# Optimization experiments

Hardware: AMD Instinct MI355X
Metric: run time of the kernel (lower is better)

Reference implementation:

```python
import jax, jax.numpy as jnp
import numpy as np

D_MODEL = 768
BATCH = 4096
RANK_DIST = [(4, 512), (8, 256), (16, 128), (32, 64), (64, 32)]


@jax.custom_vjp
def jumprelu(x):
    # hard threshold at 0 in fwd; full straight-through estimator in bwd
    return x * (x > 0.0).astype(x.dtype)


def _jr_fwd(x):
    return jumprelu(x), None


def _jr_bwd(res, g):
    return (g,)


jumprelu.defvjp(_jr_fwd, _jr_bwd)


def setup_inputs() -> dict:
    key = jax.random.key(0)
    keys = jax.random.split(key, 1 + 3 * len(RANK_DIST))
    inp = {"x": jax.random.normal(keys[0], (BATCH, D_MODEL), dtype=jnp.float32)}
    for i, (n, r) in enumerate(RANK_DIST):
        kV, kU, kE = keys[1 + 3 * i], keys[2 + 3 * i], keys[3 + 3 * i]
        scale = (1.0 / (D_MODEL * r)) ** 0.25
        inp[f"V{i}"] = scale * jax.random.normal(kV, (n, r, D_MODEL), dtype=jnp.float32)
        inp[f"U{i}"] = scale * jax.random.normal(kU, (n, D_MODEL, r), dtype=jnp.float32)
        enc = jax.random.normal(kE, (n, D_MODEL), dtype=jnp.float32)
        inp[f"enc{i}"] = enc / jnp.linalg.norm(enc, axis=1, keepdims=True)
        inp[f"b{i}"] = jnp.full((n,), -1.0, dtype=jnp.float32)
    return inp


def _group_forward(x, V, U, enc, b):
    n, r, d = V.shape
    pre = x @ enc.T - b                      # (b, n)
    gate = jumprelu(pre)                     # (b, n)
    Vx = jnp.einsum("nrd,bd->nbr", V, x)    # (n, b, r)
    # fused: UVx gated by gate then summed over transforms n
    out = jnp.einsum("ndr,nbr,bn->bd", U, Vx, gate)  # (b, d)
    u_norms = jnp.linalg.norm(U.reshape(n, -1), axis=1)
    v_norms = jnp.linalg.norm(V.reshape(n, -1), axis=1)
    frob = u_norms * v_norms / jnp.sqrt(jnp.asarray(d * r, dtype=x.dtype))
    return out, gate, frob


def reference(x, V0, U0, enc0, b0, V1, U1, enc1, b1, V2, U2, enc2, b2,
              V3, U3, enc3, b3, V4, U4, enc4, b4):
    Vs = [V0, V1, V2, V3, V4]
    Us = [U0, U1, U2, U3, U4]
    encs = [enc0, enc1, enc2, enc3, enc4]
    bs = [b0, b1, b2, b3, b4]
    output = jnp.zeros_like(x)
    total_sparsity = jnp.asarray(0.0, dtype=x.dtype)
    total_active = jnp.asarray(0.0, dtype=x.dtype)
    gate_acts = []
    for V, U, enc, b in zip(Vs, Us, encs, bs):
        g_out, gate, frob = _group_forward(x, V, U, enc, b)
        output = output + g_out
        mean_abs_gate = jnp.abs(gate).mean(axis=0)
        total_sparsity = total_sparsity + (jnp.tanh(mean_abs_gate) * frob).sum()
        total_active = total_active + (gate > 0).astype(x.dtype).sum(axis=1).mean()
        gate_acts.append(gate)
    return (output, total_sparsity, total_active, *gate_acts)
```

## Files before the change

### kernel.cpp

```cpp
#include <hip/hip_runtime.h>

#define BATCH 4096
#define DM 768
#define LTOT 10240
#define NG 124

typedef __bf16 bf16x8 __attribute__((ext_vector_type(8)));
typedef short short8 __attribute__((ext_vector_type(8)));
typedef float f32x4 __attribute__((ext_vector_type(4)));

struct Ptr5 { const float* p[5]; };

__device__ __forceinline__ unsigned short f2bf(float f) {
    unsigned u = __builtin_bit_cast(unsigned, f);
    unsigned r = (u + 0x7FFFu + ((u >> 16) & 1u)) >> 16;
    return (unsigned short)r;
}

__device__ __forceinline__ short8 pack8(float4 a, float4 b) {
    union { unsigned short u[8]; short8 s; } o;
    o.u[0] = f2bf(a.x); o.u[1] = f2bf(a.y); o.u[2] = f2bf(a.z); o.u[3] = f2bf(a.w);
    o.u[4] = f2bf(b.x); o.u[5] = f2bf(b.y); o.u[6] = f2bf(b.z); o.u[7] = f2bf(b.w);
    return o.s;
}


__global__ __launch_bounds__(256) void prep_k(const float* __restrict__ x,
                                              Ptr5 vp, Ptr5 up, Ptr5 ep, Ptr5 bp,
                                              unsigned short* __restrict__ vb,
                                              unsigned short* __restrict__ w2t,
                                              unsigned short* __restrict__ xb,
                                              float* __restrict__ gate_ws,
                                              float* __restrict__ outg,
                                              float* __restrict__ vslot,
                                              float* __restrict__ uslot,
                                              float* __restrict__ gslot,
                                              float* __restrict__ aslot) {
    const int basen[5] = {0, 4, 12, 28, 60};
    int bx = blockIdx.x;
    int tid = threadIdx.x;
    if (bx < 32) {
        __shared__ unsigned short lA[128 * 64];
        __shared__ unsigned short lB[128 * 64];
        __shared__ float sgs[128];
        __shared__ float sac;
        int wave = tid >> 6, lane = tid & 63;
        int wm = wave >> 1, wn = wave & 1;
        int lan15 = lane & 15, quad = lane >> 4;
        int sw = lan15 & 7;
        int m0 = bx * 128;
        f32x4 acc[4][4] = {};
        for (int k0 = 0; k0 < DM; k0 += 64) {
            __syncthreads();
            #pragma unroll
            for (int i = 0; i < 4; i++) {
                int gidx = i * 256 + tid;
                int row = gidx >> 3, kb = gidx & 7;
                int r7 = row & 7;
                int la = (row >> 3) * 512 + r7 * 64 + (kb ^ r7) * 8;
                int sidx = (m0 + row) * 192 + (k0 >> 2) + kb * 2;
                float4 a0 = ((const float4*)x)[sidx];
                float4 a1 = ((const float4*)x)[sidx + 1];
                *(short8*)(lA + la) = pack8(a0, a1);
                float4 b0 = {0.f, 0.f, 0.f, 0.f}, b1 = {0.f, 0.f, 0.f, 0.f};
                if (row < NG) {
                    int g = (row < 4) ? 0 : (row < 12) ? 1 : (row < 28) ? 2 :
                            (row < 60) ? 3 : 4;
                    int ni = row - basen[g];
                    int eidx = ni * 192 + (k0 >> 2) + kb * 2;
                    b0 = ((const float4*)ep.p[g])[eidx];
                    b1 = ((const float4*)ep.p[g])[eidx + 1];
                }
                *(short8*)(lB + la) = pack8(b0, b1);
            }
            __syncthreads();
            #pragma unroll
            for (int kk = 0; kk < 2; kk++) {
                int kb = kk * 4 + quad;
                int kel = (kb ^ sw) * 8;
                bf16x8 af[4], bfr[4];
                #pragma unroll
                for (int t = 0; t < 4; t++) {
                    short8 ra = *(const short8*)(lA + (wm * 64 + t * 16 + lan15) * 64 + kel);
                    short8 rb = *(const short8*)(lB + (wn * 64 + t * 16 + lan15) * 64 + kel);
                    af[t]  = __builtin_bit_cast(bf16x8, ra);
                    bfr[t] = __builtin_bit_cast(bf16x8, rb);
                }
                #pragma unroll
                for (int mt = 0; mt < 4; mt++)
                    #pragma unroll
                    for (int nt = 0; nt < 4; nt++)
                        acc[mt][nt] = __builtin_amdgcn_mfma_f32_16x16x32_bf16(
                            af[mt], bfr[nt], acc[mt][nt], 0, 0, 0);
            }
        }
        if (tid < 128) sgs[tid] = 0.f;
        if (tid == 0) sac = 0.f;
        __syncthreads();
        const size_t baseg[5] = {3145730ull, 3145730ull + 16384, 3145730ull + 49152,
                                 3145730ull + 114688, 3145730ull + 245760};
        float cnt = 0.f;
        #pragma unroll
        for (int nt = 0; nt < 4; nt++) {
            int col = wn * 64 + nt * 16 + lan15;
            float cs = 0.f;
            if (col < NG) {
                int g = (col < 4) ? 0 : (col < 12) ? 1 : (col < 28) ? 2 :
                        (col < 60) ? 3 : 4;
                int ni = col - basen[g];
                int w = 4 << g;
                float bv = bp.p[g][ni];
                #pragma unroll
                for (int mt = 0; mt < 4; mt++) {
                    int r0 = m0 + wm * 64 + mt * 16 + quad * 4;
                    #pragma unroll
                    for (int rg = 0; rg < 4; rg++) {
                        float pre = acc[mt][nt][rg] - bv;
                        float gt = pre > 0.f ? pre : 0.f;
                        gate_ws[(size_t)(r0 + rg) * NG + col] = gt;
                        outg[baseg[g] + (size_t)(r0 + rg) * w + ni] = gt;
                        cs += gt;
                        if (pre > 0.f) cnt += 1.f;
                    }
                }
                cs += __shfl_xor(cs, 16);
                cs += __shfl_xor(cs, 32);
                if (quad == 0) atomicAdd(&sgs[col], cs);
            }
        }
        #pragma unroll
        for (int off = 32; off > 0; off >>= 1) cnt += __shfl_xor(cnt, off);
        if (lane == 0) atomicAdd(&sac, cnt);
        __syncthreads();
        if (tid < NG) gslot[bx * NG + tid] = sgs[tid];
        if (tid == 0) aslot[bx] = sac;
    } else if (bx < 1952) {
        __shared__ float swave[4];
        int cb = bx - 32;
        int isV = cb < 960;
        int wb = isV ? cb : cb - 960;
        int g = wb / 192;
        int within = wb - g * 192;
        const float* src = isV ? vp.p[g] : up.p[g];
        int r = 512 >> g, lr = 9 - g;
        float ss = 0.f;
        #pragma unroll
        for (int i = 0; i < 8; i++) {
            int j = within * 2048 + i * 256 + tid;
            float4 v = ((const float4*)src)[j];
            ss += v.x*v.x + v.y*v.y + v.z*v.z + v.w*v.w;
            ushort4 o;
            o.x = f2bf(v.x); o.y = f2bf(v.y); o.z = f2bf(v.z); o.w = f2bf(v.w);
            if (isV) {
                ((ushort4*)vb)[(size_t)(g * 192 + within) * 2048 + i * 256 + tid] = o;
            } else {
                int idx = j * 4;
                int rr = idx & (r - 1);
                int t2 = idx >> lr;
                int d  = t2 % DM;
                int n  = t2 / DM;
                size_t dst = (size_t)d * LTOT + (size_t)(g << 11) + (size_t)n * r + rr;
                *(ushort4*)(w2t + dst) = o;
            }
        }
        #pragma unroll
        for (int off = 32; off > 0; off >>= 1) ss += __shfl_down(ss, off);
        if ((tid & 63) == 0) swave[tid >> 6] = ss;
        __syncthreads();
        if (tid == 0) {
            float t = (swave[0] + swave[1]) + (swave[2] + swave[3]);
            (isV ? vslot : uslot)[wb] = t;
        }
    } else {
        int base = (bx - 1952) * 2048;
        #pragma unroll
        for (int i = 0; i < 8; i++) {
            int j = base + i * 256 + tid;
            float4 v = ((const float4*)x)[j];
            ushort4 o;
            o.x = f2bf(v.x); o.y = f2bf(v.y); o.z = f2bf(v.z); o.w = f2bf(v.w);
            ((ushort4*)xb)[j] = o;
        }
    }
}

template <int ROWS, int NT>
__device__ __forceinline__ void stage(const unsigned short* __restrict__ src, int ld,
                                      unsigned short* lds, int wv, int lane) {
    int rsub = lane >> 3;
    int colb = ((lane ^ rsub) & 7) * 8;
    #pragma unroll
    for (int i = 0; i < ROWS * 8 / NT; i++) {
        int c = i * (NT / 64) + wv;
        const unsigned short* gp = src + (size_t)(c * 8 + rsub) * ld + colb;
        __builtin_amdgcn_global_load_lds((const __attribute__((address_space(1))) void*)gp,
                                         (__attribute__((address_space(3))) void*)(lds + c * 512),
                                         16, 0, 0);
    }
}

template <int BM, int BN, int NT>
__global__ __launch_bounds__(NT) void gemm_nt(const unsigned short* __restrict__ A,
                                              const unsigned short* __restrict__ Bm,
                                              int Kblk, int lda, int ldb,
                                              void* __restrict__ Cout,
                                              const float* __restrict__ gate, int ldc) {
    __shared__ unsigned short lA[BM * 64];
    __shared__ unsigned short lB[BN * 64];
    int tid = threadIdx.x, wave = tid >> 6, lane = tid & 63;
    constexpr int WN = BN / 64;
    int wm = wave / WN, wn = wave % WN;
    int m0 = blockIdx.x * BM, n0 = blockIdx.y * BN;
    A  += (size_t)m0 * lda;
    Bm += (size_t)n0 * ldb;
    f32x4 acc[4][4] = {};
    int lan15 = lane & 15, quad = lane >> 4;
    int sw = lan15 & 7;

    for (int k0 = 0; k0 < Kblk; k0 += 64) {
        stage<BM, NT>(A + k0, lda, lA, wave, lane);
        stage<BN, NT>(Bm + k0, ldb, lB, wave, lane);
        __syncthreads();
        #pragma unroll
        for (int kk = 0; kk < 2; kk++) {
            int kb = kk * 4 + quad;
            int kel = (kb ^ sw) * 8;
            bf16x8 af[4], bfr[4];
            #pragma unroll
            for (int t = 0; t < 4; t++) {
                short8 ra = *(const short8*)(lA + (size_t)(wm * 64 + t * 16 + lan15) * 64 + kel);
                short8 rb = *(const short8*)(lB + (size_t)(wn * 64 + t * 16 + lan15) * 64 + kel);
                af[t]  = __builtin_bit_cast(bf16x8, ra);
                bfr[t] = __builtin_bit_cast(bf16x8, rb);
            }
            #pragma unroll
            for (int mt = 0; mt < 4; mt++)
                #pragma unroll
                for (int nt = 0; nt < 4; nt++)
                    acc[mt][nt] = __builtin_amdgcn_mfma_f32_16x16x32_bf16(af[mt], bfr[nt],
                                                                          acc[mt][nt], 0, 0, 0);
        }
        __syncthreads();
    }

    const int basen[5] = {0, 4, 12, 28, 60};
    unsigned short* H = (unsigned short*)Cout;
    #pragma unroll
    for (int mt = 0; mt < 4; mt++) {
        __syncthreads();
        #pragma unroll
        for (int nt = 0; nt < 4; nt++) {
            int col = n0 + wn * 64 + nt * 16 + lan15;
            int g = col >> 11;
            int ngl = basen[g] + ((col & 2047) >> (9 - g));
            #pragma unroll
            for (int rg = 0; rg < 4; rg++) {
                int grow = m0 + wm * 64 + mt * 16 + quad * 4 + rg;
                float gv = gate[(size_t)grow * NG + ngl];
                lA[wave * 1024 + (quad * 4 + rg) * 64 + nt * 16 + lan15] =
                    f2bf(acc[mt][nt][rg] * gv);
            }
        }
        __syncthreads();
        #pragma unroll
        for (int i = 0; i < 2; i++) {
            int f = i * NT + tid;
            int R = f >> 5;
            int u = f & 31;
            int wv2 = ((R >> 4) << 2) + (u >> 3);
            short8 vread = *(const short8*)(lA + wv2 * 1024 + (R & 15) * 64 + (u & 7) * 8);
            int grow = m0 + (R >> 4) * 64 + mt * 16 + (R & 15);
            *(short8*)(H + (size_t)grow * ldc + n0 + u * 8) = vread;
        }
    }
}

__global__ __launch_bounds__(512, 1) void gemm2_nt(const unsigned short* __restrict__ A,
                                                   const unsigned short* __restrict__ Bm,
                                                   float* __restrict__ P) {
    __shared__ unsigned short lds[65536];
    const int tid = threadIdx.x;
    const int wave = tid >> 6, lane = tid & 63;
    const int wm = wave >> 2, wn = wave & 3;
    const int lan15 = lane & 15, quad = lane >> 4;
    const int swz = quad ^ ((lan15 >> 1) & 3);
    const int m0 = blockIdx.x * 256, n0 = blockIdx.y * 256;
    const unsigned short* Ab = A  + (size_t)m0 * LTOT + blockIdx.z * 2048;
    const unsigned short* Bb = Bm + (size_t)n0 * LTOT + blockIdx.z * 2048;
    const int srow = lane >> 2;
    const int sgr  = (lane & 3) ^ ((lane >> 3) & 3);
    const int rdA = (wm * 128 + lan15) * 32 + swz * 8;
    const int rdB = 32768 + (wn * 64 + lan15) * 32 + swz * 8;

#define STG(base_us, gb, koff) do { \
    const unsigned short* _s0 = (gb) + (size_t)(wave * 16 + srow) * LTOT + (koff) + sgr * 8; \
    const unsigned short* _s1 = (gb) + (size_t)((wave + 8) * 16 + srow) * LTOT + (koff) + sgr * 8; \
    __builtin_amdgcn_global_load_lds((const __attribute__((address_space(1))) void*)_s0, \
        (__attribute__((address_space(3))) void*)(lds + (base_us) + wave * 512), 16, 0, 0); \
    __builtin_amdgcn_global_load_lds((const __attribute__((address_space(1))) void*)_s1, \
        (__attribute__((address_space(3))) void*)(lds + (base_us) + (wave + 8) * 512), 16, 0, 0); \
} while (0)
#define STGA(buf, kh, koff) STG(((buf) * 2 + (kh)) * 8192, Ab, koff)
#define STGB(buf, kh, koff) STG(32768 + ((buf) * 2 + (kh)) * 8192, Bb, koff)

#define RDA(msub, bufkg) { \
    _Pragma("unroll") for (int t = 0; t < 4; t++) \
        af[t] = __builtin_bit_cast(bf16x8, \
            *(const short8*)(lds + (bufkg) * 8192 + rdA + ((msub) * 64 + t * 16) * 32)); }
#define RDB(bufkg) { \
    _Pragma("unroll") for (int t = 0; t < 4; t++) \
        bf[t] = __builtin_bit_cast(bf16x8, \
            *(const short8*)(lds + 32768 + (bufkg) * 8192 + rdB - 32768 + t * 512)); }
#define SYNC1 do { __builtin_amdgcn_s_barrier(); \
    asm volatile("s_waitcnt lgkmcnt(0)" ::: "memory"); \
    __builtin_amdgcn_sched_barrier(0); } while (0)
#define MM(msub) do { __builtin_amdgcn_s_setprio(1); \
    _Pragma("unroll") for (int mt = 0; mt < 4; mt++) \
        _Pragma("unroll") for (int nf = 0; nf < 4; nf++) \
            acc[(msub) * 4 + mt][nf] = __builtin_amdgcn_mfma_f32_16x16x32_bf16( \
                af[mt], bf[nf], acc[(msub) * 4 + mt][nf], 0, 0, 0); \
    __builtin_amdgcn_s_setprio(0); } while (0)
#define SYNC2 do { asm volatile("" ::: "memory"); __builtin_amdgcn_s_barrier(); \
    asm volatile("" ::: "memory"); } while (0)

    f32x4 acc[8][4] = {};
    STGA(0, 0, 0);  STGB(0, 0, 0);
    STGA(0, 1, 32); STGB(0, 1, 32);
    STGA(1, 0, 64); STGB(1, 0, 64);
    STGB(1, 1, 96);
    asm volatile("s_waitcnt vmcnt(10)" ::: "memory");
    __builtin_amdgcn_s_barrier();

    for (int i = 0; i < 32; i++) {
        const int buf = i & 1;
        bf16x8 af[4], bf[4];
        RDA(0, buf * 2 + 0); RDB(buf * 2 + 0);
        if (i + 1 < 32) STGA(buf ^ 1, 1, (i + 1) * 64 + 32);
        SYNC1; MM(0); SYNC2;
        RDA(1, buf * 2 + 0);
        if (i + 2 < 32) STGB(buf, 0, (i + 2) * 64);
        SYNC1; MM(1);
        asm volatile("s_waitcnt vmcnt(6)" ::: "memory");
        SYNC2;
        RDA(0, buf * 2 + 1); RDB(buf * 2 + 1);
        if (i + 2 < 32) STGA(buf, 0, (i + 2) * 64);
        SYNC1; MM(0); SYNC2;
        RDA(1, buf * 2 + 1);
        if (i + 2 < 32) STGB(buf, 1, (i + 2) * 64 + 32);
        SYNC1; MM(1); SYNC2;
    }
    asm volatile("s_waitcnt vmcnt(0)" ::: "memory");
#undef STG
#undef STGA
#undef STGB
#undef RDA
#undef RDB
#undef SYNC1
#undef SYNC2
#undef MM

    float* Pz = P + (size_t)blockIdx.z * ((size_t)BATCH * DM);
    #pragma unroll
    for (int mf = 0; mf < 8; mf++) {
        #pragma unroll
        for (int rg = 0; rg < 4; rg++) {
            int row = m0 + wm * 128 + mf * 16 + quad * 4 + rg;
            float* pr = Pz + (size_t)row * DM + n0 + wn * 64 + lan15;
            #pragma unroll
            for (int nf = 0; nf < 4; nf++)
                pr[nf * 16] = acc[mf][nf][rg];
        }
    }
}


__global__ __launch_bounds__(256) void reduce_k(const float4* __restrict__ P,
                                                float4* __restrict__ out, int quarter,
                                                const float* __restrict__ vslot,
                                                const float* __restrict__ uslot,
                                                const float* __restrict__ gslot,
                                                const float* __restrict__ aslot,
                                                float* __restrict__ o2) {
    int i = blockIdx.x * 256 + threadIdx.x;
    float4 a = P[i], b = P[i + quarter], c = P[i + 2 * quarter], d = P[i + 3 * quarter];
    float4 e = P[i + 4 * quarter];
    float4 o;
    o.x = ((a.x + b.x) + (c.x + d.x)) + e.x;
    o.y = ((a.y + b.y) + (c.y + d.y)) + e.y;
    o.z = ((a.z + b.z) + (c.z + d.z)) + e.z;
    o.w = ((a.w + b.w) + (c.w + d.w)) + e.w;
    out[i] = o;
    if (blockIdx.x == 0) {
        __shared__ float sh[128];
        const int basen[5] = {0, 4, 12, 28, 60};
        int t = threadIdx.x;
        if (t < 128) {
            float v = 0.f;
            if (t < NG) {
                int g = (t < 4) ? 0 : (t < 12) ? 1 : (t < 28) ? 2 : (t < 60) ? 3 : 4;
                int nloc = t - basen[g];
                int bpseg = 48 >> g;
                float vs = 0.f, us = 0.f;
                int base = g * 192 + nloc * bpseg;
                for (int j = 0; j < bpseg; j++) { vs += vslot[base + j]; us += uslot[base + j]; }
                float gs = 0.f;
                for (int bb = 0; bb < 32; bb++) gs += gslot[bb * NG + t];
                float rr = (float)(512 >> g);
                float mean = gs * (1.0f / BATCH);
                float frob = sqrtf(us * vs) / sqrtf(768.0f * rr);
                v = tanhf(mean) * frob;
            }
            sh[t] = v;
        }
        if (t == 128) {
            float asum = 0.f;
            for (int bb = 0; bb < 32; bb++) asum += aslot[bb];
            o2[1] = asum * (1.0f / BATCH);
        }
        __syncthreads();
        for (int s = 64; s > 0; s >>= 1) {
            if (threadIdx.x < s) sh[threadIdx.x] += sh[threadIdx.x + s];
            __syncthreads();
        }
        if (threadIdx.x == 0) o2[0] = sh[0];
    }
}


extern "C" void kernel_launch(void* const* d_in, const int* in_sizes, int n_in,
                              void* d_out, int out_size, void* d_ws, size_t ws_size,
                              hipStream_t stream) {
    const float* x = (const float*)d_in[0];
    Ptr5 vp, up, ep, bp;
    for (int g = 0; g < 5; g++) {
        vp.p[g] = (const float*)d_in[1 + 4 * g];
        up.p[g] = (const float*)d_in[2 + 4 * g];
        ep.p[g] = (const float*)d_in[3 + 4 * g];
        bp.p[g] = (const float*)d_in[4 + 4 * g];
    }
    float* out = (float*)d_out;
    char* ws = (char*)d_ws;
    size_t off = 0;
    unsigned short* w2t  = (unsigned short*)(ws + off); off += (size_t)LTOT * DM * 2;
    float* vslot         = (float*)(ws + off);          off += 960 * 4;
    float* uslot         = (float*)(ws + off);          off += 960 * 4;
    float* gslot         = (float*)(ws + off);          off += 32 * NG * 4;
    float* aslot         = (float*)(ws + off);          off += 32 * 4 + 256;
    unsigned short* Hg   = (unsigned short*)(ws + off); off += (size_t)BATCH * LTOT * 2;
    float* partial       = (float*)(ws + off);          off += 5ull * BATCH * DM * 4;
    unsigned short* xb      = (unsigned short*)partial;
    unsigned short* vb      = (unsigned short*)((char*)partial + (size_t)BATCH * DM * 2);
    float* gate_ws          = (float*)((char*)partial + (size_t)BATCH * DM * 2
                                                      + (size_t)LTOT * DM * 2);

    prep_k<<<dim3(2336), 256, 0, stream>>>(
        x, vp, up, ep, bp, vb, w2t, xb, gate_ws, out,
        vslot, uslot, gslot, aslot);

    gemm_nt<128, 256, 512><<<dim3(BATCH / 128, LTOT / 256, 1), 512, 0, stream>>>(
        xb, vb, DM, DM, DM, (void*)Hg, gate_ws, LTOT);
    gemm2_nt<<<dim3(BATCH / 256, DM / 256, 5), 512, 0, stream>>>(Hg, w2t, partial);
    reduce_k<<<dim3(BATCH * DM / 4 / 256), 256, 0, stream>>>(
        (const float4*)partial, (float4*)out, BATCH * DM / 4,
        vslot, uslot, gslot, aslot, out + (size_t)BATCH * DM);
}
```

Measured before the change: 329.6 us.

## Replace first GEMM with triple-buffered, interleaved load/MFMA pipelined kernel

Replaces the simple staged gemm_nt (single-buffered, full barrier per K step) for the x·V projection with a new gemm1_fg kernel. It uses a 256x128 tile, 32-wide K steps and three LDS buffers, and issues async global-to-LDS loads two steps ahead, split between MFMA halves. It adds s_setprio around the MFMAs and vmcnt-based waits, plus a drain fix in gemm2 on its last iteration. The aim is to hide memory latency and barrier stalls in the first GEMM, at the cost of more complex hand-tuned synchronisation.

```diff
diff --git a/kernel.cpp b/kernel.cpp
--- a/kernel.cpp
+++ b/kernel.cpp
@@ -184,94 +184,122 @@
     }
 }
 
-template <int ROWS, int NT>
-__device__ __forceinline__ void stage(const unsigned short* __restrict__ src, int ld,
-                                      unsigned short* lds, int wv, int lane) {
-    int rsub = lane >> 3;
-    int colb = ((lane ^ rsub) & 7) * 8;
+__global__ __launch_bounds__(512, 4) void gemm1_fg(const unsigned short* __restrict__ A,
+                                                   const unsigned short* __restrict__ Bm,
+                                                   unsigned short* __restrict__ Hg,
+                                                   const float* __restrict__ gate) {
+    __shared__ unsigned short lds[36864];
+    const int tid = threadIdx.x;
+    const int wave = tid >> 6, lane = tid & 63;
+    const int wm = wave >> 1, wn = wave & 1;
+    const int lan15 = lane & 15, quad = lane >> 4;
+    const int swz = quad ^ ((lan15 >> 1) & 3);
+    const int m0 = blockIdx.x * 256, n0 = blockIdx.y * 128;
+    const unsigned short* Ab = A  + (size_t)m0 * DM;
+    const unsigned short* Bb = Bm + (size_t)n0 * DM;
+    const int srow = lane >> 2;
+    const int sgr  = (lane & 3) ^ ((lane >> 3) & 3);
+    const int rdA0 = (wm * 64 + lan15) * 32 + swz * 8;
+    const int rdB0 = 24576 + (wn * 64 + lan15) * 32 + swz * 8;
+
+#define STA(buf, koff) do { \
+    __builtin_amdgcn_global_load_lds((const __attribute__((address_space(1))) void*)( \
+        Ab + (size_t)(wave * 16 + srow) * DM + (koff) + sgr * 8), \
+        (__attribute__((address_space(3))) void*)(lds + (buf) * 8192 + wave * 512), 16, 0, 0); \
+    __builtin_amdgcn_global_load_lds((const __attribute__((address_space(1))) void*)( \
+        Ab + (size_t)((wave + 8) * 16 + srow) * DM + (koff) + sgr * 8), \
+        (__attribute__((address_space(3))) void*)(lds + (buf) * 8192 + (wave + 8) * 512), 16, 0, 0); \
+} while (0)
+#define STB(buf, koff) \
+    __builtin_amdgcn_global_load_lds((const __attribute__((address_space(1))) void*)( \
+        Bb + (size_t)(wave * 16 + srow) * DM + (koff) + sgr * 8), \
+        (__attribute__((address_space(3))) void*)(lds + 24576 + (buf) * 4096 + wave * 512), 16, 0, 0)
+#define SYNC1 do { __builtin_amdgcn_s_barrier(); \
+    asm volatile("s_waitcnt lgkmcnt(0)" ::: "memory"); \
+    __builtin_amdgcn_sched_barrier(0); } while (0)
+#define SYNC2 do { asm volatile("" ::: "memory"); __builtin_amdgcn_s_barrier(); \
+    asm volatile("" ::: "memory"); } while (0)
+
+    f32x4 acc[4][4] = {};
+    STA(0, 0); STB(0, 0);
+    STA(1, 32); STB(1, 32);
+    asm volatile("s_waitcnt vmcnt(3)" ::: "memory");
+    __builtin_amdgcn_s_barrier();
+
+    int buf = 0;
+    for (int t = 0; t < 24; t++) {
+        int bnext = buf + 2; if (bnext >= 3) bnext -= 3;
+        bf16x8 af[4], bf[4];
+        #pragma unroll
+        for (int x = 0; x < 2; x++)
+            af[x] = __builtin_bit_cast(bf16x8, *(const short8*)(lds + buf * 8192 + rdA0 + x * 512));
+        #pragma unroll
+        for (int x = 0; x < 4; x++)
+            bf[x] = __builtin_bit_cast(bf16x8, *(const short8*)(lds + buf * 4096 + rdB0 + x * 512));
+        if (t + 2 < 24) STA(bnext, (t + 2) * 32);
+        SYNC1;
+        __builtin_amdgcn_s_setprio(1);
+        #pragma unroll
+        for (int mt = 0; mt < 2; mt++)
+            #pragma unroll
+            for (int nt = 0; nt < 4; nt++)
+                acc[mt][nt] = __builtin_amdgcn_mfma_f32_16x16x32_bf16(af[mt], bf[nt],
+                                                                     acc[mt][nt], 0, 0, 0);
+        __builtin_amdgcn_s_setprio(0);
+        SYNC2;
+        #pragma unroll
+        for (int x = 0; x < 2; x++)
+            af[2 + x] = __builtin_bit_cast(bf16x8, *(const short8*)(lds + buf * 8192 + rdA0 + (2 + x) * 512));
+        if (t + 2 < 24) STB(bnext, (t + 2) * 32);
+        SYNC1;
+        __builtin_amdgcn_s_setprio(1);
+        #pragma unroll
+        for (int mt = 2; mt < 4; mt++)
+            #pragma unroll
+            for (int nt = 0; nt < 4; nt++)
+                acc[mt][nt] = __builtin_amdgcn_mfma_f32_16x16x32_bf16(af[mt], bf[nt],
+                                                                     acc[mt][nt], 0, 0, 0);
+        __builtin_amdgcn_s_setprio(0);
+        if (t >= 22) { asm volatile("s_waitcnt vmcnt(0)" ::: "memory"); }
+        else         { asm volatile("s_waitcnt vmcnt(3)" ::: "memory"); }
+        SYNC2;
+        buf = (buf == 2) ? 0 : buf + 1;
+    }
+#undef STA
+#undef STB
+#undef SYNC1
+#undef SYNC2
+
+    const int basen[5] = {0, 4, 12, 28, 60};
     #pragma unroll
-    for (int i = 0; i < ROWS * 8 / NT; i++) {
-        int c = i * (NT / 64) + wv;
-        const unsigned short* gp = src + (size_t)(c * 8 + rsub) * ld + colb;
-        __builtin_amdgcn_global_load_lds((const __attribute__((address_space(1))) void*)gp,
-                                         (__attribute__((address_space(3))) void*)(lds + c * 512),
-                                         16, 0, 0);
-    }
-}
-
-template <int BM, int BN, int NT>
-__global__ __launch_bounds__(NT) void gemm_nt(const unsigned short* __restrict__ A,
-                                              const unsigned short* __restrict__ Bm,
-                                              int Kblk, int lda, int ldb,
-                                              void* __restrict__ Cout,
-                                              const float* __restrict__ gate, int ldc) {
-    __shared__ unsigned short lA[BM * 64];
-    __shared__ unsigned short lB[BN * 64];
-    int tid = threadIdx.x, wave = tid >> 6, lane = tid & 63;
-    constexpr int WN = BN / 64;
-    int wm = wave / WN, wn = wave % WN;
-    int m0 = blockIdx.x * BM, n0 = blockIdx.y * BN;
-    A  += (size_t)m0 * lda;
-    Bm += (size_t)n0 * ldb;
-    f32x4 acc[4][4] = {};
-    int lan15 = lane & 15, quad = lane >> 4;
-    int sw = lan15 & 7;
-
-    for (int k0 = 0; k0 < Kblk; k0 += 64) {
-        stage<BM, NT>(A + k0, lda, lA, wave, lane);
-        stage<BN, NT>(Bm + k0, ldb, lB, wave, lane);
-        __syncthreads();
-        #pragma unroll
-        for (int kk = 0; kk < 2; kk++) {
-            int kb = kk * 4 + quad;
-            int kel = (kb ^ sw) * 8;
-            bf16x8 af[4], bfr[4];
-            #pragma unroll
-            for (int t = 0; t < 4; t++) {
-                short8 ra = *(const short8*)(lA + (size_t)(wm * 64 + t * 16 + lan15) * 64 + kel);
-                short8 rb = *(const short8*)(lB + (size_t)(wn * 64 + t * 16 + lan15) * 64 + kel);
-                af[t]  = __builtin_bit_cast(bf16x8, ra);
-                bfr[t] = __builtin_bit_cast(bf16x8, rb);
-            }
-            #pragma unroll
-            for (int mt = 0; mt < 4; mt++)
-                #pragma unroll
-                for (int nt = 0; nt < 4; nt++)
-                    acc[mt][nt] = __builtin_amdgcn_mfma_f32_16x16x32_bf16(af[mt], bfr[nt],
-                                                                          acc[mt][nt], 0, 0, 0);
-        }
-        __syncthreads();
-    }
-
-    const int basen[5] = {0, 4, 12, 28, 60};
-    unsigned short* H = (unsigned short*)Cout;
-    #pragma unroll
-    for (int mt = 0; mt < 4; mt++) {
-        __syncthreads();
-        #pragma unroll
-        for (int nt = 0; nt < 4; nt++) {
-            int col = n0 + wn * 64 + nt * 16 + lan15;
+    for (int mf = 0; mf < 4; mf++) {
+        #pragma unroll
+        for (int nf = 0; nf < 4; nf++) {
+            int col = n0 + wn * 64 + nf * 16 + lan15;
             int g = col >> 11;
             int ngl = basen[g] + ((col & 2047) >> (9 - g));
             #pragma unroll
             for (int rg = 0; rg < 4; rg++) {
-                int grow = m0 + wm * 64 + mt * 16 + quad * 4 + rg;
+                int grow = m0 + wm * 64 + mf * 16 + quad * 4 + rg;
                 float gv = gate[(size_t)grow * NG + ngl];
-                lA[wave * 1024 + (quad * 4 + rg) * 64 + nt * 16 + lan15] =
-                    f2bf(acc[mt][nt][rg] * gv);
-            }
-        }
-        __syncthreads();
-        #pragma unroll
-        for (int i = 0; i < 2; i++) {
-            int f = i * NT + tid;
-            int R = f >> 5;
-            int u = f & 31;
-            int wv2 = ((R >> 4) << 2) + (u >> 3);
-            short8 vread = *(const short8*)(lA + wv2 * 1024 + (R & 15) * 64 + (u & 7) * 8);
-            int grow = m0 + (R >> 4) * 64 + mt * 16 + (R & 15);
-            *(short8*)(H + (size_t)grow * ldc + n0 + u * 8) = vread;
-        }
+                lds[wave * 1024 + (quad * 4 + rg) * 64 + nf * 16 + lan15] =
+                    f2bf(acc[mf][nf][rg] * gv);
+            }
+        }
+        asm volatile("s_waitcnt lgkmcnt(0)" ::: "memory");
+        __builtin_amdgcn_s_barrier();
+        #pragma unroll
+        for (int it = 0; it < 2; it++) {
+            int f = it * 512 + tid;
+            int R = f >> 4;
+            int u = f & 15;
+            int strip = (R >> 4) * 2 + (u >> 3);
+            short8 v = *(const short8*)(lds + strip * 1024 + (R & 15) * 64 + (u & 7) * 8);
+            int grow = m0 + (R >> 4) * 64 + mf * 16 + (R & 15);
+            *(short8*)(Hg + (size_t)grow * LTOT + n0 + u * 8) = v;
+        }
+        asm volatile("s_waitcnt lgkmcnt(0)" ::: "memory");
+        __builtin_amdgcn_s_barrier();
     }
 }
 
@@ -340,7 +368,8 @@
         RDA(1, buf * 2 + 0);
         if (i + 2 < 32) STGB(buf, 0, (i + 2) * 64);
         SYNC1; MM(1);
-        asm volatile("s_waitcnt vmcnt(6)" ::: "memory");
+        if (i == 31) { asm volatile("s_waitcnt vmcnt(0)" ::: "memory"); }
+        else         { asm volatile("s_waitcnt vmcnt(6)" ::: "memory"); }
         SYNC2;
         RDA(0, buf * 2 + 1); RDB(buf * 2 + 1);
         if (i + 2 < 32) STGA(buf, 0, (i + 2) * 64);
@@ -457,8 +486,8 @@
         x, vp, up, ep, bp, vb, w2t, xb, gate_ws, out,
         vslot, uslot, gslot, aslot);
 
-    gemm_nt<128, 256, 512><<<dim3(BATCH / 128, LTOT / 256, 1), 512, 0, stream>>>(
-        xb, vb, DM, DM, DM, (void*)Hg, gate_ws, LTOT);
+    gemm1_fg<<<dim3(BATCH / 256, LTOT / 128, 1), 512, 0, stream>>>(
+        xb, vb, Hg, gate_ws);
     gemm2_nt<<<dim3(BATCH / 256, DM / 256, 5), 512, 0, stream>>>(Hg, w2t, partial);
     reduce_k<<<dim3(BATCH * DM / 4 / 256), 256, 0, stream>>>(
         (const float4*)partial, (float4*)out, BATCH * DM / 4,
```

New measurement: 335.8 us. No clear change (+1.9%).
